# Kernel optimization log

Hardware: AMD Instinct MI355X
Metric: run time of the kernel (lower is better)

## Reference

```python
import jax, jax.numpy as jnp
import numpy as np

N = 50000      # nodes
F_IN = 256     # nfeat
HID = 64       # nhid (per-head, layer 1)
H = 4          # heads layer 1
OUT = 64       # nhid2 (layer 2, heads=1, concat=False)
E = 800000     # edges (self-loops appended in reference)
NEG_SLOPE = 0.2  # PyG GATConv default LeakyReLU slope


def setup_inputs() -> dict:
    key = jax.random.key(0)
    ks = jax.random.split(key, 10)
    x = jax.random.normal(ks[0], (N, F_IN), dtype=jnp.float32)
    adj = jax.random.randint(ks[1], (2, E), 0, N)
    s1 = 1.0 / np.sqrt(F_IN)
    s2 = 1.0 / np.sqrt(H * HID)
    W1 = (jax.random.normal(ks[2], (F_IN, H * HID), dtype=jnp.float32) * s1)
    att_src1 = jax.random.normal(ks[3], (H, HID), dtype=jnp.float32) * 0.1
    att_dst1 = jax.random.normal(ks[4], (H, HID), dtype=jnp.float32) * 0.1
    b1 = jnp.zeros((H * HID,), dtype=jnp.float32)
    W2 = (jax.random.normal(ks[5], (H * HID, OUT), dtype=jnp.float32) * s2)
    att_src2 = jax.random.normal(ks[6], (1, OUT), dtype=jnp.float32) * 0.1
    att_dst2 = jax.random.normal(ks[7], (1, OUT), dtype=jnp.float32) * 0.1
    b2 = jnp.zeros((OUT,), dtype=jnp.float32)
    return {"x": x, "adj": adj, "W1": W1, "att_src1": att_src1,
            "att_dst1": att_dst1, "b1": b1, "W2": W2, "att_src2": att_src2,
            "att_dst2": att_dst2, "b2": b2}


def _gat_conv(x, src, dst, W, a_src, a_dst, bias, heads, out_ch, concat):
    n = x.shape[0]
    h = (x @ W).reshape(n, heads, out_ch)                    # [N, H, C]
    alpha_src = jnp.einsum('nhc,hc->nh', h, a_src)           # [N, H]
    alpha_dst = jnp.einsum('nhc,hc->nh', h, a_dst)           # [N, H]
    alpha = jax.nn.leaky_relu(alpha_src[src] + alpha_dst[dst],
                              negative_slope=NEG_SLOPE)      # [E, H]
    # segment softmax over incoming edges of each dst node
    m = jax.ops.segment_max(alpha, dst, num_segments=n)      # [N, H]
    e = jnp.exp(alpha - m[dst])
    denom = jax.ops.segment_sum(e, dst, num_segments=n)      # [N, H]
    a = e / denom[dst]                                       # [E, H]
    msg = h[src] * a[:, :, None]                             # [E, H, C]
    out = jax.ops.segment_sum(msg, dst, num_segments=n)      # [N, H, C]
    if concat:
        out = out.reshape(n, heads * out_ch)
    else:
        out = out.mean(axis=1)
    return out + bias


def reference(x, adj, W1, att_src1, att_dst1, b1, W2, att_src2, att_dst2, b2):
    loops = jnp.arange(N, dtype=adj.dtype)
    src = jnp.concatenate([adj[0], loops])
    dst = jnp.concatenate([adj[1], loops])
    h = _gat_conv(x, src, dst, W1, att_src1, att_dst1, b1, H, HID, True)
    h = jax.nn.elu(h)
    out = _gat_conv(h, src, dst, W2, att_src2, att_dst2, b2, 1, OUT, False)
    return jax.nn.log_softmax(out, axis=1)
```

## Files before the change

### kernel.cpp

```cpp
#include <hip/hip_runtime.h>
#include <cstdint>
#include <cstddef>

#define NN    50000
#define EE    800000
#define SLOPE 0.2f
#define MT64  782
#define SEB   1563
#define CAP   64

typedef unsigned short ushortT;
typedef __attribute__((ext_vector_type(8))) short short8;
typedef __attribute__((ext_vector_type(4))) float floatx4;

__device__ __forceinline__ float lrelu(float x){ return x > 0.f ? x : SLOPE * x; }
__device__ __forceinline__ float eluf(float x){ return x > 0.f ? x : __expf(x) - 1.f; }
__device__ __forceinline__ ushortT f2b(float f){ unsigned u = __float_as_uint(f); u += 0x7fff + ((u >> 16) & 1); return (ushortT)(u >> 16); }
__device__ __forceinline__ float   b2f(ushortT b){ return __uint_as_float(((unsigned)b) << 16); }

__global__ __launch_bounds__(256) void castW_k(const float* __restrict__ W1, const float* __restrict__ W2,
                                               ushortT* __restrict__ W1T, ushortT* __restrict__ W2T,
                                               int* __restrict__ cnt)
{
    int k = blockIdx.x, t = threadIdx.x;
    W1T[t * 256 + k] = f2b(W1[k * 256 + t]);
    if (t < 64) W2T[t * 256 + k] = f2b(W2[k * 64 + t]);
    int i = k * 256 + t;
    if (i < NN) cnt[i] = 0;
}

__global__ __launch_bounds__(256, 3) void gemmscatter_k(const float* __restrict__ x,
                                                        const ushortT* __restrict__ W1T,
                                                        const float* __restrict__ attS,
                                                        const float* __restrict__ attD,
                                                        ushortT* __restrict__ h1b,
                                                        float* __restrict__ asrc,
                                                        float* __restrict__ adst,
                                                        const int* __restrict__ srcA,
                                                        const int* __restrict__ dstA,
                                                        int* __restrict__ cnt,
                                                        ushortT* __restrict__ esorted)
{
    if (blockIdx.x >= MT64) {
        int e0 = (blockIdx.x - MT64) * 512 + threadIdx.x;
        #pragma unroll
        for (int k = 0; k < 2; ++k) {
            int e = e0 + k * 256;
            if (e < EE) {
                int s = srcA[e], d = dstA[e];
                int r = atomicAdd(cnt + d, 1);
                if (r < CAP) esorted[d * CAP + r] = (ushortT)s;
            }
        }
        return;
    }

    const int tid  = threadIdx.x;
    const int w    = tid >> 6;
    const int lane = tid & 63;
    const int m16  = lane & 15;
    const int quad = lane >> 4;
    const int wr   = w >> 1;
    const int wc   = w & 1;
    const int rowbase = blockIdx.x * 64 + wr * 32;
    const int colbase = wc * 128;

    const long r0 = min(rowbase + m16,      NN - 1);
    const long r1 = min(rowbase + 16 + m16, NN - 1);
    const float* a0p = x + r0 * 256 + quad * 8;
    const float* a1p = x + r1 * 256 + quad * 8;
    const ushortT* bp0 = W1T + (size_t)(colbase + m16) * 256 + quad * 8;

    floatx4 acc[2][8];
    #pragma unroll
    for (int i = 0; i < 2; ++i)
        #pragma unroll
        for (int j = 0; j < 8; ++j) acc[i][j] = (floatx4){0.f, 0.f, 0.f, 0.f};

    #pragma unroll
    for (int it = 0; it < 8; ++it) {
        const int k0 = it * 32;
        float4 fa00 = *(const float4*)(a0p + k0);
        float4 fa01 = *(const float4*)(a0p + k0 + 4);
        float4 fa10 = *(const float4*)(a1p + k0);
        float4 fa11 = *(const float4*)(a1p + k0 + 4);
        uint4 fb[8];
        #pragma unroll
        for (int j = 0; j < 8; ++j)
            fb[j] = *(const uint4*)(bp0 + (size_t)j * 16 * 256 + k0);

        ushortT a16[16];
        a16[0]=f2b(fa00.x); a16[1]=f2b(fa00.y); a16[2]=f2b(fa00.z); a16[3]=f2b(fa00.w);
        a16[4]=f2b(fa01.x); a16[5]=f2b(fa01.y); a16[6]=f2b(fa01.z); a16[7]=f2b(fa01.w);
        a16[8]=f2b(fa10.x); a16[9]=f2b(fa10.y); a16[10]=f2b(fa10.z); a16[11]=f2b(fa10.w);
        a16[12]=f2b(fa11.x); a16[13]=f2b(fa11.y); a16[14]=f2b(fa11.z); a16[15]=f2b(fa11.w);
        short8 af0 = *(short8*)(a16);
        short8 af1 = *(short8*)(a16 + 8);

        #pragma unroll
        for (int j = 0; j < 8; ++j) {
            short8 bf = *(short8*)(&fb[j]);
            acc[0][j] = __builtin_amdgcn_mfma_f32_16x16x32_bf16(af0, bf, acc[0][j], 0, 0, 0);
            acc[1][j] = __builtin_amdgcn_mfma_f32_16x16x32_bf16(af1, bf, acc[1][j], 0, 0, 0);
        }
    }

    float attSv[8], attDv[8];
    #pragma unroll
    for (int j = 0; j < 8; ++j) {
        attSv[j] = attS[colbase + j * 16 + m16];
        attDv[j] = attD[colbase + j * 16 + m16];
    }

    #pragma unroll
    for (int i = 0; i < 2; ++i) {
        #pragma unroll
        for (int r = 0; r < 4; ++r) {
            int row = rowbase + i * 16 + quad * 4 + r;
            bool ok = row < NN;
            if (ok) {
                #pragma unroll
                for (int j = 0; j < 8; ++j)
                    h1b[(size_t)row * 256 + colbase + j * 16 + m16] = f2b(acc[i][j][r]);
            }
            float d0 = 0.f, d1 = 0.f, e0 = 0.f, e1 = 0.f;
            #pragma unroll
            for (int jj = 0; jj < 4; ++jj) {
                d0 += acc[i][jj][r]     * attSv[jj];
                e0 += acc[i][jj][r]     * attDv[jj];
                d1 += acc[i][jj + 4][r] * attSv[jj + 4];
                e1 += acc[i][jj + 4][r] * attDv[jj + 4];
            }
            #pragma unroll
            for (int off = 1; off < 16; off <<= 1) {
                d0 += __shfl_xor(d0, off); e0 += __shfl_xor(e0, off);
                d1 += __shfl_xor(d1, off); e1 += __shfl_xor(e1, off);
            }
            if (ok && m16 == 0) {
                int hb = row * 4 + wc * 2;
                asrc[hb] = d0; asrc[hb + 1] = d1;
                adst[hb] = e0; adst[hb + 1] = e1;
            }
        }
    }
}

__global__ __launch_bounds__(256) void gemm2_k(const ushortT* __restrict__ a2b,
                                               const ushortT* __restrict__ W2T,
                                               const float* __restrict__ attS,
                                               const float* __restrict__ attD,
                                               ushortT* __restrict__ t2b,
                                               float* __restrict__ asrc,
                                               float* __restrict__ adst)
{
    const int tid  = threadIdx.x;
    const int w    = tid >> 6;
    const int lane = tid & 63;
    const int m16  = lane & 15;
    const int quad = lane >> 4;
    const int rowbase = blockIdx.x * 64 + w * 16;

    const long r0 = min(rowbase + m16, NN - 1);
    const ushortT* ap  = a2b + r0 * 256 + quad * 8;
    const ushortT* bp0 = W2T + (size_t)m16 * 256 + quad * 8;

    floatx4 acc[4];
    #pragma unroll
    for (int j = 0; j < 4; ++j) acc[j] = (floatx4){0.f, 0.f, 0.f, 0.f};

    #pragma unroll
    for (int it = 0; it < 8; ++it) {
        const int k0 = it * 32;
        uint4 fa = *(const uint4*)(ap + k0);
        uint4 fb[4];
        #pragma unroll
        for (int j = 0; j < 4; ++j)
            fb[j] = *(const uint4*)(bp0 + (size_t)j * 16 * 256 + k0);
        short8 af = *(short8*)(&fa);
        #pragma unroll
        for (int j = 0; j < 4; ++j) {
            short8 bf = *(short8*)(&fb[j]);
            acc[j] = __builtin_amdgcn_mfma_f32_16x16x32_bf16(af, bf, acc[j], 0, 0, 0);
        }
    }

    float attSv[4], attDv[4];
    #pragma unroll
    for (int j = 0; j < 4; ++j) {
        attSv[j] = attS[j * 16 + m16];
        attDv[j] = attD[j * 16 + m16];
    }

    #pragma unroll
    for (int r = 0; r < 4; ++r) {
        int row = rowbase + quad * 4 + r;
        bool ok = row < NN;
        if (ok) {
            #pragma unroll
            for (int j = 0; j < 4; ++j)
                t2b[(size_t)row * 64 + j * 16 + m16] = f2b(acc[j][r]);
        }
        float ds = 0.f, dd = 0.f;
        #pragma unroll
        for (int j = 0; j < 4; ++j) {
            ds += acc[j][r] * attSv[j];
            dd += acc[j][r] * attDv[j];
        }
        #pragma unroll
        for (int off = 1; off < 16; off <<= 1) {
            ds += __shfl_xor(ds, off);
            dd += __shfl_xor(dd, off);
        }
        if (ok && m16 == 0) {
            asrc[row] = ds;
            adst[row] = dd;
        }
    }
}

__global__ __launch_bounds__(256) void agg1_k(const ushortT* __restrict__ esorted,
                                              const int* __restrict__ cnt,
                                              const ushortT* __restrict__ h1b,
                                              const float* __restrict__ asrc,
                                              const float* __restrict__ adst,
                                              const float* __restrict__ b1,
                                              ushortT* __restrict__ a2b)
{
    __shared__ float pbuf[4][64][4];
    __shared__ int   sbuf[4][64];
    int w = threadIdx.x >> 6;
    int lane = threadIdx.x & 63;
    int n = blockIdx.x * 4 + w;
    if (n >= NN) return;
    int start = n * CAP;
    int deg = min(cnt[n], CAP);
    float4 adv = *(const float4*)(adst + (size_t)n * 4);
    float4 asf = *(const float4*)(asrc + (size_t)n * 4);
    int h = lane >> 4;
    int c4 = lane * 4;

    float4 pself;
    pself.x = __expf(lrelu(asf.x + adv.x));
    pself.y = __expf(lrelu(asf.y + adv.y));
    pself.z = __expf(lrelu(asf.z + adv.z));
    pself.w = __expf(lrelu(asf.w + adv.w));
    float psh = (h < 2) ? (h == 0 ? pself.x : pself.y) : (h == 2 ? pself.z : pself.w);

    ushort4 hsv = *(const ushort4*)(h1b + (size_t)n * 256 + c4);
    float4 ac0 = make_float4(b2f(hsv.x) * psh, b2f(hsv.y) * psh, b2f(hsv.z) * psh, b2f(hsv.w) * psh);
    float4 ac1 = make_float4(0.f,0.f,0.f,0.f);
    float4 ac2 = make_float4(0.f,0.f,0.f,0.f);
    float4 ac3 = make_float4(0.f,0.f,0.f,0.f);
    float4 ssv = make_float4(0.f, 0.f, 0.f, 0.f);

    for (int base = 0; base < deg; base += 64) {
        int cl = min(64, deg - base);
        int i = base + lane;
        if (i < deg) {
            int s = esorted[start + i];
            float4 a = *(const float4*)(asrc + (size_t)s * 4);
            float4 pv;
            pv.x = __expf(lrelu(a.x + adv.x));
            pv.y = __expf(lrelu(a.y + adv.y));
            pv.z = __expf(lrelu(a.z + adv.z));
            pv.w = __expf(lrelu(a.w + adv.w));
            ssv.x += pv.x; ssv.y += pv.y; ssv.z += pv.z; ssv.w += pv.w;
            *(float4*)(&pbuf[w][lane][0]) = pv;
            sbuf[w][lane] = s;
        }
        __builtin_amdgcn_wave_barrier();
        int j = 0;
        for (; j + 7 < cl; j += 8) {
            float4 hv[8]; float pp[8];
            #pragma unroll
            for (int q = 0; q < 8; ++q) {
                int sq = sbuf[w][j + q];
                pp[q] = pbuf[w][j + q][h];
                ushort4 hq = *(const ushort4*)(h1b + (size_t)sq * 256 + c4);
                hv[q] = make_float4(b2f(hq.x), b2f(hq.y), b2f(hq.z), b2f(hq.w));
            }
            #pragma unroll
            for (int q = 0; q < 8; ++q) {
                float4* ac = (q & 3) == 0 ? &ac0 : (q & 3) == 1 ? &ac1 : (q & 3) == 2 ? &ac2 : &ac3;
                ac->x += hv[q].x * pp[q]; ac->y += hv[q].y * pp[q];
                ac->z += hv[q].z * pp[q]; ac->w += hv[q].w * pp[q];
            }
        }
        for (; j < cl; ++j) {
            int s0 = sbuf[w][j];
            float p0 = pbuf[w][j][h];
            ushort4 h0 = *(const ushort4*)(h1b + (size_t)s0 * 256 + c4);
            ac0.x += b2f(h0.x) * p0; ac0.y += b2f(h0.y) * p0; ac0.z += b2f(h0.z) * p0; ac0.w += b2f(h0.w) * p0;
        }
        __builtin_amdgcn_wave_barrier();
    }

    #pragma unroll
    for (int off = 1; off < 64; off <<= 1) {
        ssv.x += __shfl_xor(ssv.x, off); ssv.y += __shfl_xor(ssv.y, off);
        ssv.z += __shfl_xor(ssv.z, off); ssv.w += __shfl_xor(ssv.w, off);
    }
    float ssh = (h < 2) ? (h == 0 ? ssv.x : ssv.y) : (h == 2 ? ssv.z : ssv.w);
    float rdh = 1.f / (ssh + psh);

    float4 bv = *(const float4*)(b1 + c4);
    ushort4 o;
    o.x = f2b(eluf((ac0.x + ac1.x + ac2.x + ac3.x) * rdh + bv.x));
    o.y = f2b(eluf((ac0.y + ac1.y + ac2.y + ac3.y) * rdh + bv.y));
    o.z = f2b(eluf((ac0.z + ac1.z + ac2.z + ac3.z) * rdh + bv.z));
    o.w = f2b(eluf((ac0.w + ac1.w + ac2.w + ac3.w) * rdh + bv.w));
    *(ushort4*)(a2b + (size_t)n * 256 + c4) = o;
}

__global__ __launch_bounds__(256) void agg2_k(const ushortT* __restrict__ esorted,
                                              const int* __restrict__ cnt,
                                              const ushortT* __restrict__ t2b,
                                              const float* __restrict__ asrc,
                                              const float* __restrict__ adst,
                                              const float* __restrict__ b2,
                                              float* __restrict__ out)
{
    __shared__ float pbuf[4][64];
    __shared__ int   sbuf[4][64];
    int w = threadIdx.x >> 6;
    int lane = threadIdx.x & 63;
    int n = blockIdx.x * 4 + w;
    if (n >= NN) return;
    int start = n * CAP;
    int deg = min(cnt[n], CAP);
    float adv = adst[n];

    float pself = __expf(lrelu(asrc[n] + adv));
    float a0 = b2f(t2b[(size_t)n * 64 + lane]) * pself;
    float a1 = 0.f, a2 = 0.f, a3 = 0.f;
    float ss = 0.f;

    for (int base = 0; base < deg; base += 64) {
        int cl = min(64, deg - base);
        int i = base + lane;
        if (i < deg) {
            int s = esorted[start + i];
            float p = __expf(lrelu(asrc[s] + adv));
            ss += p;
            pbuf[w][lane] = p;
            sbuf[w][lane] = s;
        }
        __builtin_amdgcn_wave_barrier();
        int j = 0;
        for (; j + 7 < cl; j += 8) {
            float tv[8]; float pp[8];
            #pragma unroll
            for (int q = 0; q < 8; ++q) {
                int sq = sbuf[w][j + q];
                pp[q] = pbuf[w][j + q];
                tv[q] = b2f(t2b[(size_t)sq * 64 + lane]);
            }
            #pragma unroll
            for (int q = 0; q < 8; ++q) {
                float* ac = (q & 3) == 0 ? &a0 : (q & 3) == 1 ? &a1 : (q & 3) == 2 ? &a2 : &a3;
                *ac += tv[q] * pp[q];
            }
        }
        for (; j < cl; ++j) {
            a0 += b2f(t2b[(size_t)sbuf[w][j] * 64 + lane]) * pbuf[w][j];
        }
        __builtin_amdgcn_wave_barrier();
    }

    #pragma unroll
    for (int off = 1; off < 64; off <<= 1) ss += __shfl_xor(ss, off);
    float v = (a0 + a1 + a2 + a3) / (ss + pself) + b2[lane];

    float m2 = v;
    #pragma unroll
    for (int off = 32; off; off >>= 1) m2 = fmaxf(m2, __shfl_xor(m2, off));
    float ex = __expf(v - m2);
    float sm = ex;
    #pragma unroll
    for (int off = 32; off; off >>= 1) sm += __shfl_xor(sm, off);
    out[(size_t)n * 64 + lane] = v - m2 - __logf(sm);
}

extern "C" void kernel_launch(void* const* d_in, const int* in_sizes, int n_in,
                              void* d_out, int out_size, void* d_ws, size_t ws_size,
                              hipStream_t stream)
{
    const float* x   = (const float*)d_in[0];
    const int*   adj = (const int*)  d_in[1];
    const float* W1  = (const float*)d_in[2];
    const float* as1 = (const float*)d_in[3];
    const float* ad1 = (const float*)d_in[4];
    const float* b1  = (const float*)d_in[5];
    const float* W2  = (const float*)d_in[6];
    const float* as2 = (const float*)d_in[7];
    const float* ad2 = (const float*)d_in[8];
    const float* b2  = (const float*)d_in[9];
    float* out = (float*)d_out;

    const size_t szH1b = (size_t)NN * 256 * 2;
    const size_t szT2b = (size_t)NN * 64 * 2;
    const size_t szA4  = (size_t)NN * 4 * 4;
    const size_t szA1  = (size_t)NN * 4;
    const size_t szE   = (size_t)NN * CAP * 2;

    char* p = (char*)d_ws;
    ushortT* h1b  = (ushortT*)p; p += szH1b;
    ushortT* a2b  = (ushortT*)p; p += szH1b;
    ushortT* t2b  = (ushortT*)p; p += szT2b;
    ushortT* W1T  = (ushortT*)p; p += 256 * 256 * 2;
    ushortT* W2T  = (ushortT*)p; p += 64 * 256 * 2;
    float* asrc1  = (float*)p; p += szA4;
    float* adst1  = (float*)p; p += szA4;
    float* asrc2  = (float*)p; p += szA1;
    float* adst2  = (float*)p; p += szA1;
    ushortT* esorted = (ushortT*)p; p += szE;
    int* cnt      = (int*)p; p += szA1;

    const int nwb = (NN + 3) / 4;

    castW_k<<<256, 256, 0, stream>>>(W1, W2, W1T, W2T, cnt);

    gemmscatter_k<<<MT64 + SEB, 256, 0, stream>>>(x, W1T, as1, ad1, h1b, asrc1, adst1,
                                                  adj, adj + EE, cnt, esorted);

    agg1_k<<<nwb, 256, 0, stream>>>(esorted, cnt, h1b, asrc1, adst1, b1, a2b);
    gemm2_k<<<MT64, 256, 0, stream>>>(a2b, W2T, as2, ad2, t2b, asrc2, adst2);
    agg2_k<<<nwb, 256, 0, stream>>>(esorted, cnt, t2b, asrc2, adst2, b2, out);
}
```

Before: 280.8 us.

## Replace global atomic edge scatter with two-pass shared-memory binned bucketing

Edges are no longer scattered straight into per-destination slots with global atomics. A first pass has each of 512 blocks bin its edges by destination into 391 bins of 128 nodes, using LDS atomics and packed records, with a global overflow list for full bins. A new bucket kernel then gathers each bin's records into shared per-node buckets and writes contiguous esorted rows and counts. This removes the random global atomics, at the cost of an extra kernel launch, an intermediate buffer and an overflow path that every bucket block must scan.

```diff
diff --git a/kernel.cpp b/kernel.cpp
--- a/kernel.cpp
+++ b/kernel.cpp
@@ -6,8 +6,13 @@
 #define EE    800000
 #define SLOPE 0.2f
 #define MT64  782
-#define SEB   1563
 #define CAP   64
+
+#define NBIN  391
+#define PBLK  512
+#define EPB   1563
+#define BCAP  24
+#define OCAP  8192
 
 typedef unsigned short ushortT;
 typedef __attribute__((ext_vector_type(8))) short short8;
@@ -20,13 +25,12 @@
 
 __global__ __launch_bounds__(256) void castW_k(const float* __restrict__ W1, const float* __restrict__ W2,
                                                ushortT* __restrict__ W1T, ushortT* __restrict__ W2T,
-                                               int* __restrict__ cnt)
+                                               int* __restrict__ ovfcnt)
 {
     int k = blockIdx.x, t = threadIdx.x;
     W1T[t * 256 + k] = f2b(W1[k * 256 + t]);
     if (t < 64) W2T[t * 256 + k] = f2b(W2[k * 64 + t]);
-    int i = k * 256 + t;
-    if (i < NN) cnt[i] = 0;
+    if (k == 0 && t == 0) *ovfcnt = 0;
 }
 
 __global__ __launch_bounds__(256, 3) void gemmscatter_k(const float* __restrict__ x,
@@ -38,19 +42,41 @@
                                                         float* __restrict__ adst,
                                                         const int* __restrict__ srcA,
                                                         const int* __restrict__ dstA,
-                                                        int* __restrict__ cnt,
-                                                        ushortT* __restrict__ esorted)
+                                                        unsigned* __restrict__ binned,
+                                                        ushortT* __restrict__ cnt2,
+                                                        unsigned* __restrict__ ovf,
+                                                        int* __restrict__ ovfcnt)
 {
     if (blockIdx.x >= MT64) {
-        int e0 = (blockIdx.x - MT64) * 512 + threadIdx.x;
-        #pragma unroll
-        for (int k = 0; k < 2; ++k) {
-            int e = e0 + k * 256;
-            if (e < EE) {
-                int s = srcA[e], d = dstA[e];
-                int r = atomicAdd(cnt + d, 1);
-                if (r < CAP) esorted[d * CAP + r] = (ushortT)s;
-            }
+        __shared__ int      hist[NBIN];
+        __shared__ unsigned lrec[NBIN][BCAP];
+        const int blk = blockIdx.x - MT64;
+        const int tid = threadIdx.x;
+        for (int i = tid; i < NBIN; i += 256) hist[i] = 0;
+        __syncthreads();
+
+        const int e0 = blk * EPB;
+        const int e1 = min(e0 + EPB, EE);
+        for (int e = e0 + tid; e < e1; e += 256) {
+            int s = srcA[e], d = dstA[e];
+            int bin = d >> 7;
+            unsigned rec = ((unsigned)s << 7) | (unsigned)(d & 127);
+            int r = atomicAdd(&hist[bin], 1);
+            if (r < BCAP) lrec[bin][r] = rec;
+            else {
+                int o = atomicAdd(ovfcnt, 1);
+                if (o < OCAP) ovf[o] = ((unsigned)s << 16) | (unsigned)d;
+            }
+        }
+        __syncthreads();
+
+        for (int b = tid; b < NBIN; b += 256)
+            cnt2[(size_t)blk * NBIN + b] = (ushortT)min(hist[b], BCAP);
+        for (int sIdx = tid; sIdx < NBIN * BCAP; sIdx += 256) {
+            int b = sIdx / BCAP;
+            int i = sIdx - b * BCAP;
+            if (i < min(hist[b], BCAP))
+                binned[((size_t)b * PBLK + blk) * BCAP + i] = lrec[b][i];
         }
         return;
     }
@@ -142,6 +168,67 @@
                 adst[hb] = e0; adst[hb + 1] = e1;
             }
         }
+    }
+}
+
+__global__ __launch_bounds__(256) void bucket_k(const unsigned* __restrict__ binned,
+                                                const ushortT* __restrict__ cnt2,
+                                                const unsigned* __restrict__ ovf,
+                                                const int* __restrict__ ovfcnt,
+                                                ushortT* __restrict__ esorted,
+                                                int* __restrict__ cnt)
+{
+    __shared__ ushortT c2[PBLK];
+    __shared__ int     lcnt[128];
+    __shared__ ushortT lbuck[128][CAP];
+    const int b = blockIdx.x;
+    const int tid = threadIdx.x;
+
+    for (int i = tid; i < 128; i += 256) lcnt[i] = 0;
+    for (int i = tid; i < PBLK; i += 256) c2[i] = cnt2[(size_t)i * NBIN + b];
+    __syncthreads();
+
+    for (int s0 = tid; s0 < PBLK * BCAP; s0 += 1024) {
+        unsigned recs[4]; int ok[4];
+        #pragma unroll
+        for (int q = 0; q < 4; ++q) {
+            int s = s0 + q * 256;
+            int blk = s / BCAP;
+            int i = s - blk * BCAP;
+            ok[q] = (i < (int)c2[blk]);
+            recs[q] = ok[q] ? binned[((size_t)b * PBLK + blk) * BCAP + i] : 0u;
+        }
+        #pragma unroll
+        for (int q = 0; q < 4; ++q) {
+            if (ok[q]) {
+                int dl = recs[q] & 127;
+                int r = atomicAdd(&lcnt[dl], 1);
+                if (r < CAP) lbuck[dl][r] = (ushortT)(recs[q] >> 7);
+            }
+        }
+    }
+
+    int nov = *ovfcnt;
+    nov = nov > OCAP ? OCAP : nov;
+    for (int i = tid; i < nov; i += 256) {
+        unsigned rec = ovf[i];
+        int d = rec & 0xFFFF;
+        if ((d >> 7) == b) {
+            int r = atomicAdd(&lcnt[d & 127], 1);
+            if (r < CAP) lbuck[d & 127][r] = (ushortT)(rec >> 16);
+        }
+    }
+    __syncthreads();
+
+    const int nbase = b << 7;
+    if (tid < 128) {
+        int n = nbase + tid;
+        if (n < NN) cnt[n] = lcnt[tid];
+    }
+    unsigned* ed = (unsigned*)(esorted + (size_t)nbase * CAP);
+    const unsigned* ls = (const unsigned*)(&lbuck[0][0]);
+    for (int i = tid; i < 128 * (CAP / 2); i += 256) {
+        if (nbase + (i >> 5) < NN) ed[i] = ls[i];
     }
 }
 
@@ -402,6 +489,8 @@
     const size_t szA4  = (size_t)NN * 4 * 4;
     const size_t szA1  = (size_t)NN * 4;
     const size_t szE   = (size_t)NN * CAP * 2;
+    const size_t szBin = (size_t)NBIN * PBLK * BCAP * 4;
+    const size_t szC2  = (size_t)PBLK * NBIN * 2;
 
     char* p = (char*)d_ws;
     ushortT* h1b  = (ushortT*)p; p += szH1b;
@@ -415,13 +504,19 @@
     float* adst2  = (float*)p; p += szA1;
     ushortT* esorted = (ushortT*)p; p += szE;
     int* cnt      = (int*)p; p += szA1;
+    unsigned* binned = (unsigned*)p; p += szBin;
+    ushortT* cnt2 = (ushortT*)p; p += szC2;
+    unsigned* ovf = (unsigned*)p; p += (size_t)OCAP * 4;
+    int* ovfcnt   = (int*)p; p += 64;
 
     const int nwb = (NN + 3) / 4;
 
-    castW_k<<<256, 256, 0, stream>>>(W1, W2, W1T, W2T, cnt);
-
-    gemmscatter_k<<<MT64 + SEB, 256, 0, stream>>>(x, W1T, as1, ad1, h1b, asrc1, adst1,
-                                                  adj, adj + EE, cnt, esorted);
+    castW_k<<<256, 256, 0, stream>>>(W1, W2, W1T, W2T, ovfcnt);
+
+    gemmscatter_k<<<MT64 + PBLK, 256, 0, stream>>>(x, W1T, as1, ad1, h1b, asrc1, adst1,
+                                                   adj, adj + EE, binned, cnt2, ovf, ovfcnt);
+
+    bucket_k<<<NBIN, 256, 0, stream>>>(binned, cnt2, ovf, ovfcnt, esorted, cnt);
 
     agg1_k<<<nwb, 256, 0, stream>>>(esorted, cnt, h1b, asrc1, adst1, b1, a2b);
     gemm2_k<<<MT64, 256, 0, stream>>>(a2b, W2T, as2, ad2, t2b, asrc2, adst2);
```

New measurement: 289.8 us. +3.2%, slower.
